# Performance work log

Measured on AMD Instinct MI355X. Metric: run time of the kernel, lower is better.

## Reference

```python
import jax, jax.numpy as jnp
import numpy as np

B, S, D, H = 2, 2048, 1024, 16
HD = D // H


def setup_inputs() -> dict:
    key = jax.random.key(0)
    ks = jax.random.split(key, 9)
    s = 1.0 / np.sqrt(D)
    return {
        "qx": jax.random.normal(ks[0], (B, S, D), jnp.float32),
        "kx": jax.random.normal(ks[1], (B, S, D), jnp.float32),
        "vx": jax.random.normal(ks[2], (B, S, D), jnp.float32),
        "mask": jnp.tril(jnp.ones((S, S), jnp.int32))[None, None],  # [1,1,S,S] causal
        "Wq": jax.random.uniform(ks[3], (D, D), jnp.float32, -s, s),
        "bq": jax.random.uniform(ks[4], (D,), jnp.float32, -s, s),
        "Wk": jax.random.uniform(ks[5], (D, D), jnp.float32, -s, s),
        "bk": jax.random.uniform(ks[6], (D,), jnp.float32, -s, s),
        "Wv": jax.random.uniform(ks[7], (D, D), jnp.float32, -s, s),
        "bv": jax.random.uniform(ks[8], (D,), jnp.float32, -s, s),
    }


def reference(qx, kx, vx, mask, Wq, bq, Wk, bk, Wv, bv):
    bat, seq_len, d_model = qx.shape
    # torch Linear: y = x @ W.T + b
    q = qx @ Wq.T + bq
    k = kx @ Wk.T + bk
    v = vx @ Wv.T + bv
    # [b, h, s, hd]
    q = q.reshape(bat, seq_len, H, HD).transpose(0, 2, 1, 3)
    k = k.reshape(bat, seq_len, H, HD).transpose(0, 2, 1, 3)
    v = v.reshape(bat, seq_len, H, HD).transpose(0, 2, 1, 3)
    # NOTE: original scales by sqrt(d_model), not sqrt(head_dim)
    attn_weight = jnp.einsum('bhqd,bhkd->bhqk', q, k) / jnp.sqrt(
        jnp.asarray(d_model, q.dtype))
    attn_weight = jnp.where(mask == 0, -jnp.inf, attn_weight)
    attn_score = jax.nn.softmax(attn_weight, axis=-1)
    attn_output = jnp.einsum('bhqk,bhkd->bhqd', attn_score, v)
    return attn_output.transpose(0, 2, 1, 3).reshape(bat, seq_len, d_model)
```

## Files before the change

### kernel.cpp

```cpp
#include <hip/hip_runtime.h>


typedef __attribute__((ext_vector_type(8))) short short8;
typedef __attribute__((ext_vector_type(4))) short shortx4;
typedef __attribute__((ext_vector_type(4))) float floatx4;

#define NEGBIG (-1.0e30f)
#define QSCALE 0.04508422002778011f

__device__ __forceinline__ float bf2f(ushort u) {
    union { unsigned int i; float f; } x; x.i = ((unsigned int)u) << 16; return x.f;
}
__device__ __forceinline__ ushort f2bf(float f) {
    union { unsigned int i; float f; } x; x.f = f;
    return (ushort)((x.i + 0x7FFFu + ((x.i >> 16) & 1u)) >> 16);
}
__device__ __forceinline__ ushort f2bf_trunc(float f) {
    union { unsigned int i; float f; } x; x.f = f;
    return (ushort)(x.i >> 16);
}
__device__ __forceinline__ void gl_lds16(const void* g, void* l) {
    __builtin_amdgcn_global_load_lds(
        (const __attribute__((address_space(1))) unsigned int*)g,
        (__attribute__((address_space(3))) unsigned int*)l, 16, 0, 0);
}

__global__ void convert_fp32(
    const float* __restrict__ qx, const float* __restrict__ kx, const float* __restrict__ vx,
    const float* __restrict__ wq, const float* __restrict__ wk, const float* __restrict__ wv,
    const float* __restrict__ bq, const float* __restrict__ bk, const float* __restrict__ bv,
    ushort* __restrict__ dst, int* __restrict__ flag)
{
    const unsigned int* w = (const unsigned int*)qx;
    int hits = 0;
#pragma unroll
    for (int i = 0; i < 4; ++i) {
        unsigned int v = w[threadIdx.x * 4 + i];
        int e = (int)((v >> 7) & 0xFF);
        hits += (e >= 100 && e <= 135) ? 1 : 0;
    }
    __shared__ int red[4];
    for (int off = 32; off; off >>= 1) hits += __shfl_down(hits, off);
    if ((threadIdx.x & 63) == 0) red[threadIdx.x >> 6] = hits;
    __syncthreads();
    const int dt = (red[0] + red[1] + red[2] + red[3] > 512) ? 1 : 0;
    if (blockIdx.x == 0 && threadIdx.x == 0) *flag = dt;
    if (dt) return;

    const int v = blockIdx.x * 256 + threadIdx.x;
    const float* src; int off = v;
    if      (v < 1048576) { src = qx; }
    else if (v < 2097152) { src = kx; off = v - 1048576; }
    else if (v < 3145728) { src = vx; off = v - 2097152; }
    else if (v < 3407872) { src = wq; off = v - 3145728; }
    else if (v < 3670016) { src = wk; off = v - 3407872; }
    else if (v < 3932160) { src = wv; off = v - 3670016; }
    else if (v < 3932416) { src = bq; off = v - 3932160; }
    else if (v < 3932672) { src = bk; off = v - 3932416; }
    else                  { src = bv; off = v - 3932672; }
    float4 f = ((const float4*)src)[off];
    shortx4 o;
    o[0] = (short)f2bf(f.x); o[1] = (short)f2bf(f.y);
    o[2] = (short)f2bf(f.z); o[3] = (short)f2bf(f.w);
    *(shortx4*)&dst[(size_t)v * 4] = o;
}

__global__ __launch_bounds__(256, 4) void qkv_gemm(
    const void* __restrict__ Xq_, const void* __restrict__ Wq_, const void* __restrict__ bq_,
    const void* __restrict__ Xk_, const void* __restrict__ Wk_, const void* __restrict__ bk_,
    const void* __restrict__ Xv_, const void* __restrict__ Wv_, const void* __restrict__ bv_,
    const ushort* __restrict__ conv,
    ushort* __restrict__ Yq, ushort* __restrict__ Yk, ushort* __restrict__ Yv,
    const int* __restrict__ flag)
{
    const int idx = blockIdx.x;
    const int xcd = idx & 7;
    const int j   = (idx >> 3) & 7;
    const int pg  = idx >> 6;
    const int p   = pg * 8 + xcd;
    const int z   = p >> 5;
    const int m0  = (p & 31) * 128;
    const int n0  = j * 128;

    const int dt = *flag;
    const ushort* X = dt ? (const ushort*)(z == 0 ? Xq_ : z == 1 ? Xk_ : Xv_)
                         : conv + (size_t)z * 4194304;
    const ushort* W = dt ? (const ushort*)(z == 0 ? Wq_ : z == 1 ? Wk_ : Wv_)
                         : conv + 12582912 + (size_t)z * 1048576;
    const ushort* bias = dt ? (const ushort*)(z == 0 ? bq_ : z == 1 ? bk_ : bv_)
                            : conv + 15728640 + z * 1024;
    ushort* Y = (z == 0) ? Yq : (z == 1) ? Yk : Yv;
    const float oscale = (z == 0) ? QSCALE : 1.0f;

    __shared__ __align__(16) ushort As[128 * 64];
    __shared__ __align__(16) ushort Bs[128 * 64];

    const int tid  = threadIdx.x;
    const int wave = tid >> 6;
    const int lane = tid & 63;
    const int col  = lane & 15;
    const int quad = lane >> 4;
    const int wm   = (wave >> 1) * 64;
    const int wn   = (wave & 1) * 64;

    floatx4 acc[4][4] = {};

    for (int k0 = 0; k0 < 1024; k0 += 64) {
        __syncthreads();
#pragma unroll
        for (int c = 0; c < 4; ++c) {
            const int o   = c * 4096 + tid * 16;
            const int row = o >> 7;
            const int bg  = ((o >> 4) & 7) ^ (row & 7);
            gl_lds16(X + (size_t)(m0 + row) * 1024 + k0 + bg * 8, &As[o >> 1]);
            gl_lds16(W + (size_t)(n0 + row) * 1024 + k0 + bg * 8, &Bs[o >> 1]);
        }
        __syncthreads();

#pragma unroll
        for (int h = 0; h < 2; ++h) {
            short8 af[4], bf_[4];
#pragma unroll
            for (int i = 0; i < 4; ++i) {
                const int ra = wm + i * 16 + col;
                const int rb = wn + i * 16 + col;
                af[i]  = *(const short8*)&As[ra * 64 + (((h * 4 + quad) ^ (ra & 7)) * 8)];
                bf_[i] = *(const short8*)&Bs[rb * 64 + (((h * 4 + quad) ^ (rb & 7)) * 8)];
            }
#pragma unroll
            for (int i = 0; i < 4; ++i)
#pragma unroll
                for (int jj = 0; jj < 4; ++jj)
                    acc[i][jj] = __builtin_amdgcn_mfma_f32_16x16x32_bf16(af[i], bf_[jj], acc[i][jj], 0, 0, 0);
        }
    }

    if (z == 2) {
#pragma unroll
        for (int jj = 0; jj < 4; ++jj) {
            const int n = n0 + wn + jj * 16 + col;
            const float bb = bf2f(bias[n]);
#pragma unroll
            for (int i = 0; i < 4; ++i) {
                const int m = m0 + wm + i * 16 + quad * 4;
                shortx4 pk;
#pragma unroll
                for (int r = 0; r < 4; ++r) pk[r] = (short)f2bf(acc[i][jj][r] + bb);
                *(shortx4*)&Y[((size_t)(m >> 11) * 1024 + n) * 2048 + (m & 2047)] = pk;
            }
        }
    } else {
#pragma unroll
        for (int jj = 0; jj < 4; ++jj) {
            const int n = n0 + wn + jj * 16 + col;
            const float bb = bf2f(bias[n]);
#pragma unroll
            for (int i = 0; i < 4; ++i)
#pragma unroll
                for (int r = 0; r < 4; ++r) {
                    const int m = m0 + wm + i * 16 + quad * 4 + r;
                    Y[(size_t)m * 1024 + n] = f2bf((acc[i][jj][r] + bb) * oscale);
                }
        }
    }
}

#define LDP 72

__global__ __launch_bounds__(256, 4) void attn(
    const ushort* __restrict__ Q, const ushort* __restrict__ K,
    const ushort* __restrict__ Vt, void* __restrict__ O,
    const int* __restrict__ flag)
{
    const int i   = blockIdx.x;
    const int xcd = i & 7;
    const int i3  = i >> 3;
    const int run = i3 >> 5;
    const int p   = i3 & 31;
    const int qt0 = (p & 1) ? (p >> 1) : (31 - (p >> 1));
    const int qt  = (run & 1) ? (31 - qt0) : qt0;
    const int g   = xcd + 8 * run;
    const int b   = g >> 4;
    const int h   = g & 15;
    const int q0  = qt * 64;
    const int dt  = *flag;

    __shared__ __align__(16) ushort Qs[64 * 64];
    __shared__ __align__(16) ushort Ks[64 * 64];
    __shared__ __align__(16) ushort Vs[64 * 64];
    __shared__ __align__(16) ushort Ps[4][16 * LDP];

    const int tid  = threadIdx.x;
    const int wave = tid >> 6;
    const int lane = tid & 63;
    const int col  = lane & 15;
    const int quad = lane >> 4;

    const size_t qkbase = ((size_t)b * 2048) * 1024 + h * 64;
    const size_t vtbase = ((size_t)(b * 16 + h) * 64) * 2048;

    short8 ones;
#pragma unroll
    for (int ii = 0; ii < 8; ++ii) ones[ii] = (short)0x3F80;

    const int o0   = tid * 16;
    const int o1   = 4096 + tid * 16;
    const int row0 = o0 >> 7, row1 = o1 >> 7;
    const int bg0  = ((o0 >> 4) & 7) ^ (row0 & 7);
    const int bg1  = ((o1 >> 4) & 7) ^ (row1 & 7);

    gl_lds16(Q + qkbase + (size_t)(q0 + row0) * 1024 + bg0 * 8, &Qs[o0 >> 1]);
    gl_lds16(Q + qkbase + (size_t)(q0 + row1) * 1024 + bg1 * 8, &Qs[o1 >> 1]);
    gl_lds16(K + qkbase + (size_t)row0 * 1024 + bg0 * 8, &Ks[o0 >> 1]);
    gl_lds16(K + qkbase + (size_t)row1 * 1024 + bg1 * 8, &Ks[o1 >> 1]);
    gl_lds16(Vt + vtbase + (size_t)row0 * 2048 + bg0 * 8, &Vs[o0 >> 1]);
    gl_lds16(Vt + vtbase + (size_t)row1 * 2048 + bg1 * 8, &Vs[o1 >> 1]);
    __syncthreads();

    const int rq = wave * 16 + col;
    const short8 qf0 = *(const short8*)&Qs[rq * 64 + (((quad    ) ^ (col & 7)) * 8)];
    const short8 qf1 = *(const short8*)&Qs[rq * 64 + (((quad + 4) ^ (col & 7)) * 8)];

    floatx4 oacc[4] = {};
    floatx4 sacc = {};

    for (int t = 0; t <= qt; ++t) {
        floatx4 s4[4];
#pragma unroll
        for (int ct = 0; ct < 4; ++ct) {
            const int rk = ct * 16 + col;
            short8 kf0 = *(const short8*)&Ks[rk * 64 + (((quad    ) ^ (col & 7)) * 8)];
            short8 kf1 = *(const short8*)&Ks[rk * 64 + (((quad + 4) ^ (col & 7)) * 8)];
            floatx4 a = {};
            a = __builtin_amdgcn_mfma_f32_16x16x32_bf16(qf0, kf0, a, 0, 0, 0);
            a = __builtin_amdgcn_mfma_f32_16x16x32_bf16(qf1, kf1, a, 0, 0, 0);
            s4[ct] = a;
        }

        if (t == qt) {
#pragma unroll
            for (int ct = 0; ct < 4; ++ct) {
                const int kidx = ct * 16 + col;
#pragma unroll
                for (int r = 0; r < 4; ++r) {
                    const int qidx = wave * 16 + quad * 4 + r;
                    s4[ct][r] = (kidx <= qidx) ? s4[ct][r] : NEGBIG;
                }
            }
        }

#pragma unroll
        for (int ct = 0; ct < 4; ++ct)
#pragma unroll
            for (int r = 0; r < 4; ++r) {
                float pv = __builtin_exp2f(s4[ct][r]);
                Ps[wave][(quad * 4 + r) * LDP + ct * 16 + col] = f2bf_trunc(pv);
            }

        short8 pf0 = *(const short8*)&Ps[wave][col * LDP + quad * 8];
        short8 pf1 = *(const short8*)&Ps[wave][col * LDP + 32 + quad * 8];

        sacc = __builtin_amdgcn_mfma_f32_16x16x32_bf16(pf0, ones, sacc, 0, 0, 0);
        sacc = __builtin_amdgcn_mfma_f32_16x16x32_bf16(pf1, ones, sacc, 0, 0, 0);

#pragma unroll
        for (int ct = 0; ct < 4; ++ct) {
            const int rv = ct * 16 + col;
            short8 vf0 = *(const short8*)&Vs[rv * 64 + (((quad    ) ^ (rv & 7)) * 8)];
            short8 vf1 = *(const short8*)&Vs[rv * 64 + (((quad + 4) ^ (rv & 7)) * 8)];
            oacc[ct] = __builtin_amdgcn_mfma_f32_16x16x32_bf16(pf0, vf0, oacc[ct], 0, 0, 0);
            oacc[ct] = __builtin_amdgcn_mfma_f32_16x16x32_bf16(pf1, vf1, oacc[ct], 0, 0, 0);
        }

        if (t < qt) {
            const int kv1 = (t + 1) * 64;
            __syncthreads();
            gl_lds16(K + qkbase + (size_t)(kv1 + row0) * 1024 + bg0 * 8, &Ks[o0 >> 1]);
            gl_lds16(K + qkbase + (size_t)(kv1 + row1) * 1024 + bg1 * 8, &Ks[o1 >> 1]);
            gl_lds16(Vt + vtbase + (size_t)row0 * 2048 + kv1 + bg0 * 8, &Vs[o0 >> 1]);
            gl_lds16(Vt + vtbase + (size_t)row1 * 2048 + kv1 + bg1 * 8, &Vs[o1 >> 1]);
            __syncthreads();
        }
    }

#pragma unroll
    for (int r = 0; r < 4; ++r) {
        const float inv = 1.0f / sacc[r];
        const int q = q0 + wave * 16 + quad * 4 + r;
#pragma unroll
        for (int ct = 0; ct < 4; ++ct) {
            const float v = oacc[ct][r] * inv;
            const size_t oidx = ((size_t)b * 2048 + q) * 1024 + h * 64 + ct * 16 + col;
            if (dt) ((ushort*)O)[oidx] = f2bf(v);
            else    ((float*)O)[oidx]  = v;
        }
    }
}

extern "C" void kernel_launch(void* const* d_in, const int* in_sizes, int n_in,
                              void* d_out, int out_size, void* d_ws, size_t ws_size,
                              hipStream_t stream) {
    const void* qx = d_in[0];
    const void* kx = d_in[1];
    const void* vx = d_in[2];
    const void* Wq = d_in[4]; const void* bq = d_in[5];
    const void* Wk = d_in[6]; const void* bk = d_in[7];
    const void* Wv = d_in[8]; const void* bv = d_in[9];

    int*    flag = (int*)d_ws;
    ushort* conv = (ushort*)((char*)d_ws + 256);
    ushort* Qw   = (ushort*)((char*)d_ws + 256 + 31463424);
    ushort* Kw   = Qw + (size_t)4096 * 1024;
    ushort* Vtw  = Kw + (size_t)4096 * 1024;

    convert_fp32<<<15363, 256, 0, stream>>>(
        (const float*)qx, (const float*)kx, (const float*)vx,
        (const float*)Wq, (const float*)Wk, (const float*)Wv,
        (const float*)bq, (const float*)bk, (const float*)bv, conv, flag);

    qkv_gemm<<<768, 256, 0, stream>>>(qx, Wq, bq, kx, Wk, bk, vx, Wv, bv,
                                      conv, Qw, Kw, Vtw, flag);

    attn<<<1024, 256, 0, stream>>>(Qw, Kw, Vtw, d_out, flag);
}
```

Measured before the change: 195.9 us.

## Give each attention wave 32 query rows with two waves per block

The attention kernel now runs 2 waves of 64 threads per block instead of 4. Each wave handles 32 query rows, so every K and V fragment read from LDS feeds two MFMA row tiles instead of one. The goal is to halve LDS fragment traffic per MFMA and cut the number of block-wide syncs per unit of work. In exchange each wave holds more registers (doubled accumulators and fragments), there are fewer waves per block to hide latency, and each thread now issues twice as many global-to-LDS loads.

```diff
diff --git a/kernel.cpp b/kernel.cpp
--- a/kernel.cpp
+++ b/kernel.cpp
@@ -167,7 +167,7 @@
 
 #define LDP 72
 
-__global__ __launch_bounds__(256, 4) void attn(
+__global__ __launch_bounds__(128, 2) void attn(
     const ushort* __restrict__ Q, const ushort* __restrict__ K,
     const ushort* __restrict__ Vt, void* __restrict__ O,
     const int* __restrict__ flag)
@@ -188,13 +188,14 @@
     __shared__ __align__(16) ushort Qs[64 * 64];
     __shared__ __align__(16) ushort Ks[64 * 64];
     __shared__ __align__(16) ushort Vs[64 * 64];
-    __shared__ __align__(16) ushort Ps[4][16 * LDP];
+    __shared__ __align__(16) ushort Ps[2][32 * LDP];
 
     const int tid  = threadIdx.x;
     const int wave = tid >> 6;
     const int lane = tid & 63;
     const int col  = lane & 15;
     const int quad = lane >> 4;
+    const int wq0  = wave * 32;
 
     const size_t qkbase = ((size_t)b * 2048) * 1024 + h * 64;
     const size_t vtbase = ((size_t)(b * 16 + h) * 64) * 2048;
@@ -203,98 +204,132 @@
 #pragma unroll
     for (int ii = 0; ii < 8; ++ii) ones[ii] = (short)0x3F80;
 
-    const int o0   = tid * 16;
-    const int o1   = 4096 + tid * 16;
-    const int row0 = o0 >> 7, row1 = o1 >> 7;
-    const int bg0  = ((o0 >> 4) & 7) ^ (row0 & 7);
-    const int bg1  = ((o1 >> 4) & 7) ^ (row1 & 7);
-
-    gl_lds16(Q + qkbase + (size_t)(q0 + row0) * 1024 + bg0 * 8, &Qs[o0 >> 1]);
-    gl_lds16(Q + qkbase + (size_t)(q0 + row1) * 1024 + bg1 * 8, &Qs[o1 >> 1]);
-    gl_lds16(K + qkbase + (size_t)row0 * 1024 + bg0 * 8, &Ks[o0 >> 1]);
-    gl_lds16(K + qkbase + (size_t)row1 * 1024 + bg1 * 8, &Ks[o1 >> 1]);
-    gl_lds16(Vt + vtbase + (size_t)row0 * 2048 + bg0 * 8, &Vs[o0 >> 1]);
-    gl_lds16(Vt + vtbase + (size_t)row1 * 2048 + bg1 * 8, &Vs[o1 >> 1]);
+    int srow[4], sbg[4], soff[4];
+#pragma unroll
+    for (int c = 0; c < 4; ++c) {
+        const int o = c * 2048 + tid * 16;
+        srow[c] = o >> 7;
+        sbg[c]  = ((o >> 4) & 7) ^ (srow[c] & 7);
+        soff[c] = o >> 1;
+    }
+
+#pragma unroll
+    for (int c = 0; c < 4; ++c) {
+        gl_lds16(Q + qkbase + (size_t)(q0 + srow[c]) * 1024 + sbg[c] * 8, &Qs[soff[c]]);
+        gl_lds16(K + qkbase + (size_t)srow[c] * 1024 + sbg[c] * 8, &Ks[soff[c]]);
+        gl_lds16(Vt + vtbase + (size_t)srow[c] * 2048 + sbg[c] * 8, &Vs[soff[c]]);
+    }
     __syncthreads();
 
-    const int rq = wave * 16 + col;
-    const short8 qf0 = *(const short8*)&Qs[rq * 64 + (((quad    ) ^ (col & 7)) * 8)];
-    const short8 qf1 = *(const short8*)&Qs[rq * 64 + (((quad + 4) ^ (col & 7)) * 8)];
-
-    floatx4 oacc[4] = {};
-    floatx4 sacc = {};
+    short8 qf[2][2];
+#pragma unroll
+    for (int ii = 0; ii < 2; ++ii) {
+        const int rq = wq0 + ii * 16 + col;
+#pragma unroll
+        for (int c = 0; c < 2; ++c)
+            qf[ii][c] = *(const short8*)&Qs[rq * 64 + (((c * 4 + quad) ^ (rq & 7)) * 8)];
+    }
+
+    floatx4 oacc[2][4] = {};
+    floatx4 sacc[2] = {};
 
     for (int t = 0; t <= qt; ++t) {
-        floatx4 s4[4];
+        short8 kf[4][2];
 #pragma unroll
         for (int ct = 0; ct < 4; ++ct) {
             const int rk = ct * 16 + col;
-            short8 kf0 = *(const short8*)&Ks[rk * 64 + (((quad    ) ^ (col & 7)) * 8)];
-            short8 kf1 = *(const short8*)&Ks[rk * 64 + (((quad + 4) ^ (col & 7)) * 8)];
-            floatx4 a = {};
-            a = __builtin_amdgcn_mfma_f32_16x16x32_bf16(qf0, kf0, a, 0, 0, 0);
-            a = __builtin_amdgcn_mfma_f32_16x16x32_bf16(qf1, kf1, a, 0, 0, 0);
-            s4[ct] = a;
-        }
+#pragma unroll
+            for (int c = 0; c < 2; ++c)
+                kf[ct][c] = *(const short8*)&Ks[rk * 64 + (((c * 4 + quad) ^ (rk & 7)) * 8)];
+        }
+
+        floatx4 s4[2][4];
+#pragma unroll
+        for (int ii = 0; ii < 2; ++ii)
+#pragma unroll
+            for (int ct = 0; ct < 4; ++ct) {
+                floatx4 a = {};
+                a = __builtin_amdgcn_mfma_f32_16x16x32_bf16(qf[ii][0], kf[ct][0], a, 0, 0, 0);
+                a = __builtin_amdgcn_mfma_f32_16x16x32_bf16(qf[ii][1], kf[ct][1], a, 0, 0, 0);
+                s4[ii][ct] = a;
+            }
 
         if (t == qt) {
 #pragma unroll
-            for (int ct = 0; ct < 4; ++ct) {
-                const int kidx = ct * 16 + col;
+            for (int ii = 0; ii < 2; ++ii)
+#pragma unroll
+                for (int ct = 0; ct < 4; ++ct) {
+                    const int kidx = ct * 16 + col;
+#pragma unroll
+                    for (int r = 0; r < 4; ++r) {
+                        const int qidx = wq0 + ii * 16 + quad * 4 + r;
+                        s4[ii][ct][r] = (kidx <= qidx) ? s4[ii][ct][r] : NEGBIG;
+                    }
+                }
+        }
+
+#pragma unroll
+        for (int ii = 0; ii < 2; ++ii)
+#pragma unroll
+            for (int ct = 0; ct < 4; ++ct)
 #pragma unroll
                 for (int r = 0; r < 4; ++r) {
-                    const int qidx = wave * 16 + quad * 4 + r;
-                    s4[ct][r] = (kidx <= qidx) ? s4[ct][r] : NEGBIG;
+                    float pv = __builtin_exp2f(s4[ii][ct][r]);
+                    Ps[wave][(ii * 16 + quad * 4 + r) * LDP + ct * 16 + col] = f2bf_trunc(pv);
                 }
-            }
-        }
-
-#pragma unroll
-        for (int ct = 0; ct < 4; ++ct)
-#pragma unroll
-            for (int r = 0; r < 4; ++r) {
-                float pv = __builtin_exp2f(s4[ct][r]);
-                Ps[wave][(quad * 4 + r) * LDP + ct * 16 + col] = f2bf_trunc(pv);
-            }
-
-        short8 pf0 = *(const short8*)&Ps[wave][col * LDP + quad * 8];
-        short8 pf1 = *(const short8*)&Ps[wave][col * LDP + 32 + quad * 8];
-
-        sacc = __builtin_amdgcn_mfma_f32_16x16x32_bf16(pf0, ones, sacc, 0, 0, 0);
-        sacc = __builtin_amdgcn_mfma_f32_16x16x32_bf16(pf1, ones, sacc, 0, 0, 0);
-
+
+        short8 pf[2][2];
+#pragma unroll
+        for (int ii = 0; ii < 2; ++ii) {
+            pf[ii][0] = *(const short8*)&Ps[wave][(ii * 16 + col) * LDP + quad * 8];
+            pf[ii][1] = *(const short8*)&Ps[wave][(ii * 16 + col) * LDP + 32 + quad * 8];
+        }
+        short8 vf[4][2];
 #pragma unroll
         for (int ct = 0; ct < 4; ++ct) {
             const int rv = ct * 16 + col;
-            short8 vf0 = *(const short8*)&Vs[rv * 64 + (((quad    ) ^ (rv & 7)) * 8)];
-            short8 vf1 = *(const short8*)&Vs[rv * 64 + (((quad + 4) ^ (rv & 7)) * 8)];
-            oacc[ct] = __builtin_amdgcn_mfma_f32_16x16x32_bf16(pf0, vf0, oacc[ct], 0, 0, 0);
-            oacc[ct] = __builtin_amdgcn_mfma_f32_16x16x32_bf16(pf1, vf1, oacc[ct], 0, 0, 0);
+#pragma unroll
+            for (int c = 0; c < 2; ++c)
+                vf[ct][c] = *(const short8*)&Vs[rv * 64 + (((c * 4 + quad) ^ (rv & 7)) * 8)];
+        }
+
+#pragma unroll
+        for (int ii = 0; ii < 2; ++ii) {
+            sacc[ii] = __builtin_amdgcn_mfma_f32_16x16x32_bf16(pf[ii][0], ones, sacc[ii], 0, 0, 0);
+            sacc[ii] = __builtin_amdgcn_mfma_f32_16x16x32_bf16(pf[ii][1], ones, sacc[ii], 0, 0, 0);
+#pragma unroll
+            for (int ct = 0; ct < 4; ++ct) {
+                oacc[ii][ct] = __builtin_amdgcn_mfma_f32_16x16x32_bf16(pf[ii][0], vf[ct][0], oacc[ii][ct], 0, 0, 0);
+                oacc[ii][ct] = __builtin_amdgcn_mfma_f32_16x16x32_bf16(pf[ii][1], vf[ct][1], oacc[ii][ct], 0, 0, 0);
+            }
         }
 
         if (t < qt) {
             const int kv1 = (t + 1) * 64;
             __syncthreads();
-            gl_lds16(K + qkbase + (size_t)(kv1 + row0) * 1024 + bg0 * 8, &Ks[o0 >> 1]);
-            gl_lds16(K + qkbase + (size_t)(kv1 + row1) * 1024 + bg1 * 8, &Ks[o1 >> 1]);
-            gl_lds16(Vt + vtbase + (size_t)row0 * 2048 + kv1 + bg0 * 8, &Vs[o0 >> 1]);
-            gl_lds16(Vt + vtbase + (size_t)row1 * 2048 + kv1 + bg1 * 8, &Vs[o1 >> 1]);
+#pragma unroll
+            for (int c = 0; c < 4; ++c) {
+                gl_lds16(K + qkbase + (size_t)(kv1 + srow[c]) * 1024 + sbg[c] * 8, &Ks[soff[c]]);
+                gl_lds16(Vt + vtbase + (size_t)srow[c] * 2048 + kv1 + sbg[c] * 8, &Vs[soff[c]]);
+            }
             __syncthreads();
         }
     }
 
 #pragma unroll
-    for (int r = 0; r < 4; ++r) {
-        const float inv = 1.0f / sacc[r];
-        const int q = q0 + wave * 16 + quad * 4 + r;
-#pragma unroll
-        for (int ct = 0; ct < 4; ++ct) {
-            const float v = oacc[ct][r] * inv;
-            const size_t oidx = ((size_t)b * 2048 + q) * 1024 + h * 64 + ct * 16 + col;
-            if (dt) ((ushort*)O)[oidx] = f2bf(v);
-            else    ((float*)O)[oidx]  = v;
-        }
-    }
+    for (int ii = 0; ii < 2; ++ii)
+#pragma unroll
+        for (int r = 0; r < 4; ++r) {
+            const float inv = 1.0f / sacc[ii][r];
+            const int q = q0 + wq0 + ii * 16 + quad * 4 + r;
+#pragma unroll
+            for (int ct = 0; ct < 4; ++ct) {
+                const float v = oacc[ii][ct][r] * inv;
+                const size_t oidx = ((size_t)b * 2048 + q) * 1024 + h * 64 + ct * 16 + col;
+                if (dt) ((ushort*)O)[oidx] = f2bf(v);
+                else    ((float*)O)[oidx]  = v;
+            }
+        }
 }
 
 extern "C" void kernel_launch(void* const* d_in, const int* in_sizes, int n_in,
@@ -321,5 +356,5 @@
     qkv_gemm<<<768, 256, 0, stream>>>(qx, Wq, bq, kx, Wk, bk, vx, Wv, bv,
                                       conv, Qw, Kw, Vtw, flag);
 
-    attn<<<1024, 256, 0, stream>>>(Qw, Kw, Vtw, d_out, flag);
-}
+    attn<<<1024, 128, 0, stream>>>(Qw, Kw, Vtw, d_out, flag);
+}
```

Result: slower. 212.1 us (+8.3%).
